# Optimization experiments

Hardware: AMD Instinct MI355X
Metric: run time of the kernel (lower is better)

## Reference

```python
import jax, jax.numpy as jnp
import numpy as np

OUT = (7, 7, 7)      # output_size (D_out, H_out, W_out)
SCALE = 1.0          # spatial_scale


def setup_inputs() -> dict:
    key = jax.random.key(0)
    k1, k2 = jax.random.split(key)
    B, C, D, H, W = 2, 256, 64, 64, 64
    N = 512
    features = jax.random.normal(k1, (B, C, D, H, W), dtype=jnp.float32)
    p = jax.random.uniform(k2, (B, N, 6), dtype=jnp.float32) * 63.0
    lo = jnp.minimum(p[..., :3], p[..., 3:])
    hi = jnp.maximum(p[..., :3], p[..., 3:])
    proposals = jnp.concatenate([lo, hi], axis=-1)  # (B, N, 6) valid boxes
    return {"features": features, "proposals": proposals}


def _trilinear(vol, gz, gy, gx):
    # vol: (C, D, H, W); gz/gy/gx: (Do, Ho, Wo) voxel-space coords.
    # grid_sample(mode='bilinear', padding_mode='zeros', align_corners=True)
    C, D, H, W = vol.shape
    z0f, y0f, x0f = jnp.floor(gz), jnp.floor(gy), jnp.floor(gx)
    wz, wy, wx = gz - z0f, gy - y0f, gx - x0f
    z0, y0, x0 = z0f.astype(jnp.int32), y0f.astype(jnp.int32), x0f.astype(jnp.int32)

    def gather(zi, yi, xi):
        valid = (zi >= 0) & (zi < D) & (yi >= 0) & (yi < H) & (xi >= 0) & (xi < W)
        v = vol[:, jnp.clip(zi, 0, D - 1), jnp.clip(yi, 0, H - 1), jnp.clip(xi, 0, W - 1)]
        return v * valid.astype(vol.dtype)[None]  # (C, Do, Ho, Wo)

    out = jnp.zeros((C,) + gz.shape, dtype=vol.dtype)
    for dz in (0, 1):
        for dy in (0, 1):
            for dx in (0, 1):
                w = ((wz if dz else 1.0 - wz)
                     * (wy if dy else 1.0 - wy)
                     * (wx if dx else 1.0 - wx))
                out = out + gather(z0 + dz, y0 + dy, x0 + dx) * w[None]
    return out


def reference(features, proposals):
    # features: (B, C, D, H, W); proposals: (B, N, 6) [x1,y1,z1,x2,y2,z2]
    B, C, D, H, W = features.shape
    Do, Ho, Wo = OUT

    def one_roi(vol, prop):
        p = prop * SCALE
        x1, y1, z1, x2, y2, z2 = p[0], p[1], p[2], p[3], p[4], p[5]
        zc = jnp.linspace(z1, z2, Do)
        yc = jnp.linspace(y1, y2, Ho)
        xc = jnp.linspace(x1, x2, Wo)
        gz, gy, gx = jnp.meshgrid(zc, yc, xc, indexing='ij')  # (Do,Ho,Wo)
        return _trilinear(vol, gz, gy, gx)  # (C, Do, Ho, Wo)

    per_batch = jax.vmap(lambda vol, props: jax.vmap(lambda p: one_roi(vol, p))(props))
    out = per_batch(features, proposals)  # (B, N, C, Do, Ho, Wo)
    return out.reshape(B * proposals.shape[1], C, Do, Ho, Wo)
```

## Files before the change

kernel.cpp:

```cpp
#include <hip/hip_runtime.h>
#include <hip/hip_fp16.h>


#define B_      2
#define C_      256
#define N_      512
#define NENT    (N_ * 7)
#define SP      66
#define PLANE_S (64 * SP)
#define THREADS 1024
#define GROUPS  20
#define REC_F_BASE 128
#define WS_NEEDED ((size_t)REC_F_BASE * 4 + (size_t)B_ * NENT * 8 * 4)

typedef _Float16 h2v __attribute__((ext_vector_type(2)));

__device__ __forceinline__ float gcoord(float lo, float hi, int i) {
    return lo + (hi - lo) * (1.0f / 6.0f) * (float)i;
}

__device__ __forceinline__ uint32_t pkrtz(float a, float b) {
    auto h = __builtin_amdgcn_cvt_pkrtz(a, b);
    return __builtin_bit_cast(uint32_t, h);
}

__device__ __forceinline__ float xlerp(uint32_t pkv, uint32_t pkw) {
#if __has_builtin(__builtin_amdgcn_fdot2)
    return __builtin_amdgcn_fdot2(__builtin_bit_cast(h2v, pkv),
                                  __builtin_bit_cast(h2v, pkw), 0.0f, false);
#else
    h2v v = __builtin_bit_cast(h2v, pkv);
    h2v w = __builtin_bit_cast(h2v, pkw);
    return (float)v[0] * (float)w[0] + (float)v[1] * (float)w[1];
#endif
}

__global__ __launch_bounds__(256) void bucket_kernel(
    const float* __restrict__ props, int* __restrict__ wsi, float* __restrict__ wsf)
{
    int b = blockIdx.x;
    __shared__ int counts[63];
    __shared__ int starts[64];
    __shared__ int cursors[63];
    int tid = threadIdx.x;
    if (tid < 63) counts[tid] = 0;
    __syncthreads();
    for (int e = tid; e < NENT; e += 256) {
        int n = e / 7, iz = e - n * 7;
        const float* pr = props + (size_t)(b * N_ + n) * 6;
        float gz = gcoord(pr[2], pr[5], iz);
        int z0 = min(max((int)gz, 0), 62);
        atomicAdd(&counts[z0], 1);
    }
    __syncthreads();
    if (tid == 0) {
        int s = 0;
        for (int k = 0; k < 63; ++k) { starts[k] = s; s += counts[k]; }
        starts[63] = s;
    }
    __syncthreads();
    if (tid < 63) cursors[tid] = starts[tid];
    __syncthreads();
    for (int e = tid; e < NENT; e += 256) {
        int n = e / 7, iz = e - n * 7;
        const float* pr = props + (size_t)(b * N_ + n) * 6;
        float x1p = pr[0], y1p = pr[1], z1p = pr[2];
        float x2p = pr[3], y2p = pr[4], z2p = pr[5];
        float gz = gcoord(z1p, z2p, iz);
        int z0 = min(max((int)gz, 0), 62);
        float wz = gz - (float)z0;
        int pos = atomicAdd(&cursors[z0], 1);
        int off = (b * N_ + n) * (C_ * 343) + iz * 49;
        float* r = wsf + REC_F_BASE + (size_t)(b * NENT + pos) * 8;
        r[0] = x1p; r[1] = (x2p - x1p) * (1.0f / 6.0f);
        r[2] = y1p; r[3] = (y2p - y1p) * (1.0f / 6.0f);
        r[4] = wz;  r[5] = __int_as_float(off);
        r[6] = 0.0f; r[7] = 0.0f;
    }
    if (tid < 64) wsi[b * 64 + tid] = starts[tid];
}

__global__ __launch_bounds__(THREADS, 8) void roialign3d_slice_kernel(
    const float* __restrict__ feat,
    const int* __restrict__ wsi,
    const float* __restrict__ wsf,
    float* __restrict__ out)
{
    __shared__ __align__(16) uint32_t pk[4 * PLANE_S];
    __shared__ int ldsStarts[64];

    int s = blockIdx.x;
    int b = s >> 8;
    int c = s & 255;
    const float* vol = feat + (size_t)s * (64 * 64 * 64);
    int tid = threadIdx.x;

    if (tid < 64) ldsStarts[tid] = wsi[b * 64 + tid];
    int swb = (tid >> 4) * SP + ((tid & 15) << 2);

#define STAGE_WRITE(slotBase, v, v4) do {                                   \
        uint2 w0 = make_uint2(pkrtz((v).x, (v).y), pkrtz((v).y, (v).z));    \
        uint2 w1 = make_uint2(pkrtz((v).z, (v).w), pkrtz((v).w, (v4)));     \
        *(uint2*)&pk[(slotBase) + swb]     = w0;                            \
        *(uint2*)&pk[(slotBase) + swb + 2] = w1;                            \
    } while (0)

    float4 v0   = *(const float4*)(vol + (tid << 2));
    float4 v1   = *(const float4*)(vol + 1 * 4096 + (tid << 2));
    float4 stgA = *(const float4*)(vol + 2 * 4096 + (tid << 2));
    {
        float a4 = __shfl_down(v0.x, 1);
        float b4 = __shfl_down(v1.x, 1);
        STAGE_WRITE(0 * PLANE_S, v0, a4);
        STAGE_WRITE(1 * PLANE_S, v1, b4);
    }
    __syncthreads();

    int g = tid / 49;
    int p = tid - g * 49;
    int iy = p / 7;
    float fx = (float)(p - iy * 7);
    float fy = (float)iy;
    bool active = (g < GROUPS);

    float* outc = out + (size_t)c * 343;
    const float4* recs = (const float4*)(wsf + REC_F_BASE);
    const int rbase = b * NENT;

    #pragma unroll 1
    for (int z = 0; z < 63; ++z) {
        int aA = (z & 3) * PLANE_S;
        int aB = ((z + 1) & 3) * PLANE_S;
        int aW = ((z + 2) & 3) * PLANE_S;

        int base = ldsStarts[z];
        int myCnt = active ? (ldsStarts[z + 1] - base) : 0;
        int roff = rbase + base;

        int e = g;
        float4 rAn, rBn;
        uint32_t pw, q0, q1, q2, q3;
        float wym, wzm; int offm;
        if (e < myCnt) {
            float4 rA1 = recs[(size_t)(roff + e) * 2];
            float4 rB1 = recs[(size_t)(roff + e) * 2 + 1];
            if (e + GROUPS < myCnt) {
                rAn = recs[(size_t)(roff + e + GROUPS) * 2];
                rBn = recs[(size_t)(roff + e + GROUPS) * 2 + 1];
            }
            float gx = fmaf(rA1.y, fx, rA1.x);
            float gy = fmaf(rA1.w, fy, rA1.z);
            int x0 = (int)gx, y0 = (int)gy;
            float wx = __builtin_amdgcn_fractf(gx);
            wym = __builtin_amdgcn_fractf(gy);
            pw = pkrtz(1.0f - wx, wx);
            wzm = rB1.x; offm = __float_as_int(rB1.y);
            int sl = y0 * SP + x0;
            q0 = pk[aA + sl]; q1 = pk[aA + sl + SP];
            q2 = pk[aB + sl]; q3 = pk[aB + sl + SP];
        }
        __builtin_amdgcn_sched_barrier(0);
        float4 stgB;
        if (z <= 60)
            stgB = *(const float4*)(vol + (size_t)(z + 3) * 4096 + (tid << 2));

        while (e < myCnt) {
            int e1 = e + GROUPS;
            int e2 = e1 + GROUPS;
            uint32_t pwc = pw, c0 = q0, c1 = q1, c2 = q2, c3 = q3;
            float wyc = wym, wzc = wzm; int offc = offm;
            if (e1 < myCnt) {
                float gx = fmaf(rAn.y, fx, rAn.x);
                float gy = fmaf(rAn.w, fy, rAn.z);
                int x0 = (int)gx, y0 = (int)gy;
                float wx = __builtin_amdgcn_fractf(gx);
                wym = __builtin_amdgcn_fractf(gy);
                pw = pkrtz(1.0f - wx, wx);
                wzm = rBn.x; offm = __float_as_int(rBn.y);
                int sl = y0 * SP + x0;
                q0 = pk[aA + sl]; q1 = pk[aA + sl + SP];
                q2 = pk[aB + sl]; q3 = pk[aB + sl + SP];
            }
            if (e2 < myCnt) {
                rAn = recs[(size_t)(roff + e2) * 2];
                rBn = recs[(size_t)(roff + e2) * 2 + 1];
            }
            float c00 = xlerp(c0, pwc);
            float c01 = xlerp(c1, pwc);
            float c10 = xlerp(c2, pwc);
            float c11 = xlerp(c3, pwc);
            float d0 = fmaf(c01 - c00, wyc, c00);
            float d1 = fmaf(c11 - c10, wyc, c10);
            outc[offc + p] = fmaf(d1 - d0, wzc, d0);
            e = e1;
        }

        if (z <= 61) {
            float a4 = __shfl_down(stgA.x, 1);
            STAGE_WRITE(aW, stgA, a4);
        }
        __syncthreads();
        stgA = stgB;
    }
#undef STAGE_WRITE
}

__global__ __launch_bounds__(128) void roialign3d_fallback(
    const float* __restrict__ feat, const float* __restrict__ props,
    float* __restrict__ out)
{
    int bid = blockIdx.x;
    int xcd = bid & 7;
    int j   = bid >> 3;
    int s   = xcd + ((j >> 9) << 3);
    int n   = j & 511;
    int b   = s >> 8;
    int c   = s & 255;
    const float* prop = props + ((size_t)(b * N_ + n)) * 6;
    float x1p = prop[0], y1p = prop[1], z1p = prop[2];
    float x2p = prop[3], y2p = prop[4], z2p = prop[5];
    float sx = (x2p - x1p) * (1.0f / 6.0f);
    float sy = (y2p - y1p) * (1.0f / 6.0f);
    float sz = (z2p - z1p) * (1.0f / 6.0f);
    const float* vol = feat + (size_t)s * (64 * 64 * 64);
    float* o = out + ((size_t)(b * N_ + n) * C_ + c) * 343;
    for (int p = threadIdx.x; p < 343; p += 128) {
        int iz = p / 49, r = p - iz * 49, iy = r / 7, ix = r - iy * 7;
        float gx = x1p + sx * ix, gy = y1p + sy * iy, gz = z1p + sz * iz;
        int x0 = (int)gx, y0 = (int)gy, z0 = (int)gz;
        float wx = gx - x0, wy = gy - y0, wz = gz - z0;
        int x1 = min(x0 + 1, 63), y1 = min(y0 + 1, 63), z1 = min(z0 + 1, 63);
        const float* p00 = vol + ((z0 * 64 + y0) << 6);
        const float* p01 = vol + ((z0 * 64 + y1) << 6);
        const float* p10 = vol + ((z1 * 64 + y0) << 6);
        const float* p11 = vol + ((z1 * 64 + y1) << 6);
        float c00 = p00[x0] + (p00[x1] - p00[x0]) * wx;
        float c01 = p01[x0] + (p01[x1] - p01[x0]) * wx;
        float c10 = p10[x0] + (p10[x1] - p10[x0]) * wx;
        float c11 = p11[x0] + (p11[x1] - p11[x0]) * wx;
        float d0 = c00 + (c01 - c00) * wy;
        float d1 = c10 + (c11 - c10) * wy;
        o[p] = d0 + (d1 - d0) * wz;
    }
}

extern "C" void kernel_launch(void* const* d_in, const int* in_sizes, int n_in,
                              void* d_out, int out_size, void* d_ws, size_t ws_size,
                              hipStream_t stream) {
    const float* feat  = (const float*)d_in[0];
    const float* props = (const float*)d_in[1];
    float* out = (float*)d_out;

    if (ws_size < WS_NEEDED) {
        roialign3d_fallback<<<B_ * C_ * N_, 128, 0, stream>>>(feat, props, out);
        return;
    }
    int*   wsi = (int*)d_ws;
    float* wsf = (float*)d_ws;
    bucket_kernel<<<B_, 256, 0, stream>>>(props, wsi, wsf);
    roialign3d_slice_kernel<<<B_ * C_, THREADS, 0, stream>>>(feat, wsi, wsf, out);
}
```

Measured before the change: 299.3 us.

## Split per-channel z-sweep into independent 3-slice chunk blocks

Replaces the per-(batch,channel) block that sweeps all 63 z-slices with a rolling 4-plane LDS pipeline by 21 independent blocks per channel. Each block loads 4 planes once, syncs once, then processes the records whose z0 falls in its 3-slice chunk, using a z0 index now stored in the record. This removes the serial per-slice barriers and gives the GPU far more blocks to schedule. In exchange each plane boundary is loaded twice (4 planes per 3 slices) and the overlap of loads with compute inside a block is lost.

```diff
diff --git a/kernel.cpp b/kernel.cpp
--- a/kernel.cpp
+++ b/kernel.cpp
@@ -8,6 +8,8 @@
 #define NENT    (N_ * 7)
 #define SP      66
 #define PLANE_S (64 * SP)
+#define CHUNK   3
+#define NCHUNK  21
 #define THREADS 1024
 #define GROUPS  20
 #define REC_F_BASE 128
@@ -75,134 +77,107 @@
         r[0] = x1p; r[1] = (x2p - x1p) * (1.0f / 6.0f);
         r[2] = y1p; r[3] = (y2p - y1p) * (1.0f / 6.0f);
         r[4] = wz;  r[5] = __int_as_float(off);
-        r[6] = 0.0f; r[7] = 0.0f;
+        r[6] = __int_as_float(z0); r[7] = 0.0f;
     }
     if (tid < 64) wsi[b * 64 + tid] = starts[tid];
 }
 
-__global__ __launch_bounds__(THREADS, 8) void roialign3d_slice_kernel(
+__global__ __launch_bounds__(THREADS, 8) void roialign3d_chunk_kernel(
     const float* __restrict__ feat,
     const int* __restrict__ wsi,
     const float* __restrict__ wsf,
     float* __restrict__ out)
 {
     __shared__ __align__(16) uint32_t pk[4 * PLANE_S];
-    __shared__ int ldsStarts[64];
-
-    int s = blockIdx.x;
+
+    int bid = blockIdx.x;
+    int s = bid & 511;
+    int k = bid >> 9;
     int b = s >> 8;
     int c = s & 255;
-    const float* vol = feat + (size_t)s * (64 * 64 * 64);
+    int zlo = k * CHUNK;
+    const float* vol = feat + (size_t)s * 262144 + (size_t)zlo * 4096;
     int tid = threadIdx.x;
 
-    if (tid < 64) ldsStarts[tid] = wsi[b * 64 + tid];
+    int base = wsi[b * 64 + zlo];
+    int end  = wsi[b * 64 + zlo + CHUNK];
+
+    float4 v0 = *(const float4*)(vol + 0 * 4096 + (tid << 2));
+    float4 v1 = *(const float4*)(vol + 1 * 4096 + (tid << 2));
+    float4 v2 = *(const float4*)(vol + 2 * 4096 + (tid << 2));
+    float4 v3 = *(const float4*)(vol + 3 * 4096 + (tid << 2));
+
+    int g = tid / 49;
+    int p = tid - g * 49;
+    int iy = p / 7;
+    float fx = (float)(p - iy * 7);
+    float fy = (float)iy;
+    const float4* recs = (const float4*)(wsf + REC_F_BASE);
+    const int rbase = b * NENT;
+    int myEnd = (g < GROUPS) ? end : base;
+    int e = base + g;
+    float4 rA, rB, rAn, rBn;
+    if (e < myEnd) {
+        rA = recs[(size_t)(rbase + e) * 2];
+        rB = recs[(size_t)(rbase + e) * 2 + 1];
+        if (e + GROUPS < myEnd) {
+            rAn = recs[(size_t)(rbase + e + GROUPS) * 2];
+            rBn = recs[(size_t)(rbase + e + GROUPS) * 2 + 1];
+        }
+    }
+
     int swb = (tid >> 4) * SP + ((tid & 15) << 2);
-
 #define STAGE_WRITE(slotBase, v, v4) do {                                   \
         uint2 w0 = make_uint2(pkrtz((v).x, (v).y), pkrtz((v).y, (v).z));    \
         uint2 w1 = make_uint2(pkrtz((v).z, (v).w), pkrtz((v).w, (v4)));     \
         *(uint2*)&pk[(slotBase) + swb]     = w0;                            \
         *(uint2*)&pk[(slotBase) + swb + 2] = w1;                            \
     } while (0)
-
-    float4 v0   = *(const float4*)(vol + (tid << 2));
-    float4 v1   = *(const float4*)(vol + 1 * 4096 + (tid << 2));
-    float4 stgA = *(const float4*)(vol + 2 * 4096 + (tid << 2));
     {
-        float a4 = __shfl_down(v0.x, 1);
-        float b4 = __shfl_down(v1.x, 1);
-        STAGE_WRITE(0 * PLANE_S, v0, a4);
-        STAGE_WRITE(1 * PLANE_S, v1, b4);
-    }
-    __syncthreads();
-
-    int g = tid / 49;
-    int p = tid - g * 49;
-    int iy = p / 7;
-    float fx = (float)(p - iy * 7);
-    float fy = (float)iy;
-    bool active = (g < GROUPS);
+        float a0 = __shfl_down(v0.x, 1);
+        float a1 = __shfl_down(v1.x, 1);
+        float a2 = __shfl_down(v2.x, 1);
+        float a3 = __shfl_down(v3.x, 1);
+        STAGE_WRITE(0 * PLANE_S, v0, a0);
+        STAGE_WRITE(1 * PLANE_S, v1, a1);
+        STAGE_WRITE(2 * PLANE_S, v2, a2);
+        STAGE_WRITE(3 * PLANE_S, v3, a3);
+    }
+#undef STAGE_WRITE
+    __syncthreads();
 
     float* outc = out + (size_t)c * 343;
-    const float4* recs = (const float4*)(wsf + REC_F_BASE);
-    const int rbase = b * NENT;
-
-    #pragma unroll 1
-    for (int z = 0; z < 63; ++z) {
-        int aA = (z & 3) * PLANE_S;
-        int aB = ((z + 1) & 3) * PLANE_S;
-        int aW = ((z + 2) & 3) * PLANE_S;
-
-        int base = ldsStarts[z];
-        int myCnt = active ? (ldsStarts[z + 1] - base) : 0;
-        int roff = rbase + base;
-
-        int e = g;
-        float4 rAn, rBn;
-        uint32_t pw, q0, q1, q2, q3;
-        float wym, wzm; int offm;
-        if (e < myCnt) {
-            float4 rA1 = recs[(size_t)(roff + e) * 2];
-            float4 rB1 = recs[(size_t)(roff + e) * 2 + 1];
-            if (e + GROUPS < myCnt) {
-                rAn = recs[(size_t)(roff + e + GROUPS) * 2];
-                rBn = recs[(size_t)(roff + e + GROUPS) * 2 + 1];
-            }
-            float gx = fmaf(rA1.y, fx, rA1.x);
-            float gy = fmaf(rA1.w, fy, rA1.z);
-            int x0 = (int)gx, y0 = (int)gy;
-            float wx = __builtin_amdgcn_fractf(gx);
-            wym = __builtin_amdgcn_fractf(gy);
-            pw = pkrtz(1.0f - wx, wx);
-            wzm = rB1.x; offm = __float_as_int(rB1.y);
-            int sl = y0 * SP + x0;
-            q0 = pk[aA + sl]; q1 = pk[aA + sl + SP];
-            q2 = pk[aB + sl]; q3 = pk[aB + sl + SP];
+    while (e < myEnd) {
+        float gx = fmaf(rA.y, fx, rA.x);
+        float gy = fmaf(rA.w, fy, rA.z);
+        int x0 = (int)gx, y0 = (int)gy;
+        float wx = __builtin_amdgcn_fractf(gx);
+        float wy = __builtin_amdgcn_fractf(gy);
+        uint32_t pw = pkrtz(1.0f - wx, wx);
+        float wz = rB.x;
+        int offc = __float_as_int(rB.y);
+        int lz = __float_as_int(rB.z) - zlo;
+        int sl = lz * PLANE_S + y0 * SP + x0;
+        uint32_t q0 = pk[sl],           q1 = pk[sl + SP];
+        uint32_t q2 = pk[sl + PLANE_S], q3 = pk[sl + PLANE_S + SP];
+
+        float4 tA = rAn, tB = rBn;
+        int e2 = e + 2 * GROUPS;
+        if (e2 < myEnd) {
+            rAn = recs[(size_t)(rbase + e2) * 2];
+            rBn = recs[(size_t)(rbase + e2) * 2 + 1];
         }
-        __builtin_amdgcn_sched_barrier(0);
-        float4 stgB;
-        if (z <= 60)
-            stgB = *(const float4*)(vol + (size_t)(z + 3) * 4096 + (tid << 2));
-
-        while (e < myCnt) {
-            int e1 = e + GROUPS;
-            int e2 = e1 + GROUPS;
-            uint32_t pwc = pw, c0 = q0, c1 = q1, c2 = q2, c3 = q3;
-            float wyc = wym, wzc = wzm; int offc = offm;
-            if (e1 < myCnt) {
-                float gx = fmaf(rAn.y, fx, rAn.x);
-                float gy = fmaf(rAn.w, fy, rAn.z);
-                int x0 = (int)gx, y0 = (int)gy;
-                float wx = __builtin_amdgcn_fractf(gx);
-                wym = __builtin_amdgcn_fractf(gy);
-                pw = pkrtz(1.0f - wx, wx);
-                wzm = rBn.x; offm = __float_as_int(rBn.y);
-                int sl = y0 * SP + x0;
-                q0 = pk[aA + sl]; q1 = pk[aA + sl + SP];
-                q2 = pk[aB + sl]; q3 = pk[aB + sl + SP];
-            }
-            if (e2 < myCnt) {
-                rAn = recs[(size_t)(roff + e2) * 2];
-                rBn = recs[(size_t)(roff + e2) * 2 + 1];
-            }
-            float c00 = xlerp(c0, pwc);
-            float c01 = xlerp(c1, pwc);
-            float c10 = xlerp(c2, pwc);
-            float c11 = xlerp(c3, pwc);
-            float d0 = fmaf(c01 - c00, wyc, c00);
-            float d1 = fmaf(c11 - c10, wyc, c10);
-            outc[offc + p] = fmaf(d1 - d0, wzc, d0);
-            e = e1;
-        }
-
-        if (z <= 61) {
-            float a4 = __shfl_down(stgA.x, 1);
-            STAGE_WRITE(aW, stgA, a4);
-        }
-        __syncthreads();
-        stgA = stgB;
-    }
-#undef STAGE_WRITE
+
+        float c00 = xlerp(q0, pw);
+        float c01 = xlerp(q1, pw);
+        float c10 = xlerp(q2, pw);
+        float c11 = xlerp(q3, pw);
+        float d0 = fmaf(c01 - c00, wy, c00);
+        float d1 = fmaf(c11 - c10, wy, c10);
+        outc[offc + p] = fmaf(d1 - d0, wz, d0);
+
+        e += GROUPS; rA = tA; rB = tB;
+    }
 }
 
 __global__ __launch_bounds__(128) void roialign3d_fallback(
@@ -258,5 +233,5 @@
     int*   wsi = (int*)d_ws;
     float* wsf = (float*)d_ws;
     bucket_kernel<<<B_, 256, 0, stream>>>(props, wsi, wsf);
-    roialign3d_slice_kernel<<<B_ * C_, THREADS, 0, stream>>>(feat, wsi, wsf, out);
-}
+    roialign3d_chunk_kernel<<<NCHUNK * 512, THREADS, 0, stream>>>(feat, wsi, wsf, out);
+}
```

New measurement: 290.4 us. 3.0% less time.
